# Performance work log

Hardware: AMD Instinct MI355X
Metric: run time of the kernel (lower is better)

The kernel has to match this reference:

```python
import jax, jax.numpy as jnp
import numpy as np

DIM = 256
DIM_HEAD = 32
HEADS = DIM // DIM_HEAD
SCALE = DIM_HEAD ** -0.5


def setup_inputs() -> dict:
    key = jax.random.key(0)
    ks = jax.random.split(key, 8)
    D1 = DIM + 1
    s = 1.0 / np.sqrt(D1)
    x = jax.random.normal(ks[0], (2, 32, 32, 8, 8, D1), dtype=jnp.float32)
    Wqv = jax.random.normal(ks[1], (D1, DIM), dtype=jnp.float32) * s
    Wkv = jax.random.normal(ks[2], (D1, DIM), dtype=jnp.float32) * s
    Wvv = jax.random.normal(ks[3], (D1, DIM), dtype=jnp.float32) * s
    Wqd = jax.random.normal(ks[4], (D1, 1), dtype=jnp.float32) * s
    Wkd = jax.random.normal(ks[5], (D1, 1), dtype=jnp.float32) * s
    Wvd = jax.random.normal(ks[6], (D1, 1), dtype=jnp.float32) * s
    Wout = jax.random.normal(ks[7], (D1, D1), dtype=jnp.float32) * s
    return {"x": x, "Wqv": Wqv, "Wkv": Wkv, "Wvv": Wvv,
            "Wqd": Wqd, "Wkd": Wkd, "Wvd": Wvd, "Wout": Wout}


def reference(x, Wqv, Wkv, Wvv, Wqd, Wkd, Wvd, Wout):
    b, gx, gy, w1, w2, D1 = x.shape
    B = b * gx * gy          # number of windows
    n = w1 * w2              # tokens per window
    h, dh = HEADS, DIM_HEAD
    xf = x.reshape(B, n, D1)

    def split_heads(t, nh, d):
        # (B, n, nh*d) -> (B, nh, n, d)
        return t.reshape(B, n, nh, d).transpose(0, 2, 1, 3)

    qv = split_heads(xf @ Wqv, h, dh) * SCALE
    kv = split_heads(xf @ Wkv, h, dh)
    vv = split_heads(xf @ Wvv, h, dh)
    qd = split_heads(xf @ Wqd, 1, 1) * SCALE
    kd = split_heads(xf @ Wkd, 1, 1)
    vd = split_heads(xf @ Wvd, 1, 1)

    sim_v = jnp.einsum('bhid,bhjd->bhij', qv, kv)          # (B, h, n, n)
    sim_d = jnp.einsum('bhid,bhjd->bhij', qd, kd)          # (B, 1, n, n)
    sim_m = sim_v * jax.nn.sigmoid(sim_d)                  # depth-gated scores

    attn_v = jax.nn.softmax(sim_m, axis=-1)                # (B, h, n, n)
    attn_d = jax.nn.softmax(jnp.sum(sim_m, axis=1, keepdims=True), axis=-1)  # (B,1,n,n)

    out_v = jnp.einsum('bhij,bhjd->bhid', attn_v, vv)      # (B, h, n, dh)
    out_d = jnp.einsum('bhij,bhjd->bhid', attn_d, vd)      # (B, 1, n, 1)

    out_v = out_v.transpose(0, 2, 1, 3).reshape(B, n, h * dh)  # (B, n, dim)
    out_d = out_d.transpose(0, 2, 1, 3).reshape(B, n, 1)       # (B, n, 1)

    out = jnp.concatenate([out_v, out_d], axis=-1) @ Wout      # (B, n, dim+1)
    return out.reshape(b, gx, gy, w1, w2, D1)
```

## Files before the change

kernel.cpp:

```cpp
#include <hip/hip_runtime.h>


#define D1    257
#define NTOK  64
#define KT    9
#define NT_CAT 49
#define NT_OUT 17
#define SCALE 0.17677669529663687f

#define XS2_OFF 0
#define QS2_OFF 36864
#define KS2_OFF 71680
#define VS2_OFF 104448
#define DS2_OFF 137216
#define QD2_OFF 153856
#define KD2_OFF 154112
#define VD2_OFF 154368
#define LDS2    154624
#define AT_STRIDE 68
#define DS_STRIDE 65

#define XS_OFF    0
#define XS_STRIDE 296
#define OC_STRIDE 296
#define QS_OFF    37888
#define QK_STRIDE 264
#define KS_OFF    72704
#define VS_OFF    106496
#define DS_OFF    139264
#define QD_OFF    155904
#define KD_OFF    156160
#define VD_OFF    156416
#define LDS_SIZE  156672

#define WCAT_ELEMS (KT * NT_CAT * 512)
#define WOUT_ELEMS (KT * NT_OUT * 512)
#define XWIN_ELEMS (36 * 512)

using bf16x8 = __attribute__((ext_vector_type(8))) short;
using s16x4  = __attribute__((ext_vector_type(4))) short;
using f32x4  = __attribute__((ext_vector_type(4))) float;

__device__ __forceinline__ short f2b(float f) {
  unsigned u = __float_as_uint(f);
  u = (u + 0x7FFFu + ((u >> 16) & 1u)) >> 16;
  return (short)u;
}

__device__ __forceinline__ f32x4 mfma16(bf16x8 a, bf16x8 b, f32x4 c) {
  return __builtin_amdgcn_mfma_f32_16x16x32_bf16(a, b, c, 0, 0, 0);
}

__global__ void prep_weights(const float* __restrict__ Wqv, const float* __restrict__ Wkv,
                             const float* __restrict__ Wvv, const float* __restrict__ Wqd,
                             const float* __restrict__ Wkd, const float* __restrict__ Wvd,
                             const float* __restrict__ Wout,
                             short* __restrict__ wcatp, short* __restrict__ woutp) {
  int idx = blockIdx.x * 256 + threadIdx.x;
  if (idx < WCAT_ELEMS) {
    int j = idx & 7, lane = (idx >> 3) & 63, rest = idx >> 9;
    int nt = rest % NT_CAT, kt = rest / NT_CAT;
    int k = 32 * kt + (lane >> 4) * 8 + j;
    int n = 16 * nt + (lane & 15);
    float v = 0.f;
    if (k < D1) {
      if (n < 256)       v = Wqv[k * 256 + n] * SCALE;
      else if (n < 512)  v = Wkv[k * 256 + (n - 256)];
      else if (n < 768)  v = Wvv[k * 256 + (n - 512)];
      else if (n == 768) v = Wqd[k] * SCALE;
      else if (n == 769) v = Wkd[k];
      else if (n == 770) v = Wvd[k];
    }
    wcatp[idx] = f2b(v);
  } else {
    int i2 = idx - WCAT_ELEMS;
    int j = i2 & 7, lane = (i2 >> 3) & 63, rest = i2 >> 9;
    int nt = rest % NT_OUT, kt = rest / NT_OUT;
    int k = 32 * kt + (lane >> 4) * 8 + j;
    int n = 16 * nt + (lane & 15);
    float v = (k < D1 && n < D1) ? Wout[k * D1 + n] : 0.f;
    woutp[i2] = f2b(v);
  }
}

__global__ void prep_x(const float* __restrict__ x, short* __restrict__ xbf, int win0) {
  int i = blockIdx.x * 256 + threadIdx.x;
  int widx = blockIdx.y;
  int j = i & 7, lane = (i >> 3) & 63, frag = i >> 9;
  int kt = frag >> 2, mt = frag & 3;
  int m = lane & 15, q = lane >> 4;
  int row = 16 * mt + m;
  int col = 32 * kt + 8 * q + j;
  float v = 0.f;
  if (col < D1)
    v = x[((size_t)(win0 + widx) * NTOK + row) * D1 + col];
  xbf[(size_t)widx * XWIN_ELEMS + i] = f2b(v);
}

__global__ __launch_bounds__(1024)
void vda_attn2(const short* __restrict__ xbf, const short* __restrict__ wcatp,
               const short* __restrict__ woutp, float* __restrict__ out, int win0) {
  extern __shared__ char smem[];
  short* xs   = (short*)(smem + XS2_OFF);
  short* qs   = (short*)(smem + QS2_OFF);
  short* ks   = (short*)(smem + KS2_OFF);
  short* vs   = (short*)(smem + VS2_OFF);
  float* dsum = (float*)(smem + DS2_OFF);
  float* qd_s = (float*)(smem + QD2_OFF);
  float* kd_s = (float*)(smem + KD2_OFF);
  float* vd_s = (float*)(smem + VD2_OFF);
  short* oc = xs;

  const int tid  = threadIdx.x;
  const int lane = tid & 63;
  const int w    = tid >> 6;
  const int m    = lane & 15;
  const int q    = lane >> 4;
  const int q8   = q * 8;
  const int widx = blockIdx.x;
  const int win  = win0 + widx;

  for (int i = tid; i < 64 * DS_STRIDE; i += 1024) dsum[i] = 0.f;
  {
    const int4* src = (const int4*)(xbf + (size_t)widx * XWIN_ELEMS);
    int4* dst = (int4*)xs;
    for (int i = tid; i < 2304; i += 1024) dst[i] = src[i];
  }
  __syncthreads();

  {
    f32x4 acc[4][4];
#pragma unroll
    for (int t = 0; t < 4; ++t)
#pragma unroll
      for (int mt = 0; mt < 4; ++mt) acc[t][mt] = f32x4{0.f, 0.f, 0.f, 0.f};

    for (int kt = 0; kt < KT; ++kt) {
      bf16x8 af[4];
#pragma unroll
      for (int mt = 0; mt < 4; ++mt)
        af[mt] = *(const bf16x8*)&xs[(kt * 4 + mt) * 512 + lane * 8];
#pragma unroll
      for (int t = 0; t < 4; ++t) {
        int nt = w + 16 * t;
        if (nt < NT_CAT) {
          bf16x8 bfr = *(const bf16x8*)(wcatp + ((size_t)(kt * NT_CAT + nt) * 64 + lane) * 8);
#pragma unroll
          for (int mt = 0; mt < 4; ++mt)
            acc[t][mt] = mfma16(af[mt], bfr, acc[t][mt]);
        }
      }
    }
    {
      int cq = (2 * w + (m >> 3)) & 3;
      int jj = m & 7;
      int fb = (w >> 1) * 4;
#pragma unroll
      for (int mt = 0; mt < 4; ++mt)
#pragma unroll
        for (int r = 0; r < 4; ++r)
          qs[(fb + mt) * 512 + (cq * 16 + 4 * q + r) * 8 + jj] = f2b(acc[0][mt][r]);
#pragma unroll
      for (int mt = 0; mt < 4; ++mt)
#pragma unroll
        for (int r = 0; r < 4; ++r)
          ks[(fb + mt) * 512 + (cq * 16 + 4 * q + r) * 8 + jj] = f2b(acc[1][mt][r]);
#pragma unroll
      for (int mt = 0; mt < 4; ++mt) {
        int frag = w * 2 + (mt >> 1);
        int q2 = (2 * mt + (q >> 1)) & 3;
        int j0 = 4 * (q & 1);
        s16x4 pk;
#pragma unroll
        for (int r = 0; r < 4; ++r) pk[r] = f2b(acc[2][mt][r]);
        *(s16x4*)&vs[frag * 512 + (q2 * 16 + m) * 8 + j0] = pk;
      }
      if (w == 0 && m < 3) {
        float* dst = (m == 0) ? qd_s : (m == 1) ? kd_s : vd_s;
#pragma unroll
        for (int mt = 0; mt < 4; ++mt)
#pragma unroll
          for (int r = 0; r < 4; ++r)
            dst[16 * mt + 4 * q + r] = acc[3][mt][r];
      }
    }
  }
  __syncthreads();

  const int rw = w & 3;
  const int hp = w >> 2;

  bf16x8 aq[2];
#pragma unroll
  for (int hh = 0; hh < 2; ++hh)
    aq[hh] = *(const bf16x8*)&qs[(((2 * hp + hh) * 4 + rw)) * 512 + lane * 8];

  float gate[4][4], ssum[4][4];
  {
    float qd_r[4], kd_c[4];
#pragma unroll
    for (int r = 0; r < 4; ++r) qd_r[r] = qd_s[16 * rw + 4 * q + r];
#pragma unroll
    for (int nt = 0; nt < 4; ++nt) kd_c[nt] = kd_s[16 * nt + m];
#pragma unroll
    for (int nt = 0; nt < 4; ++nt)
#pragma unroll
      for (int r = 0; r < 4; ++r) {
        float t = qd_r[r] * kd_c[nt];
        gate[nt][r] = 1.f / (1.f + __expf(-t));
        ssum[nt][r] = 0.f;
      }
  }
  __syncthreads();

  if (hp == 0) {
    int4 z4; z4.x = 0; z4.y = 0; z4.z = 0; z4.w = 0;
    ((int4*)(oc + 32 * 512))[rw * 64 + lane] = z4;
  }

  short* atw = (short*)(smem + QS2_OFF) + w * (16 * AT_STRIDE);

#pragma unroll
  for (int hh = 0; hh < 2; ++hh) {
    int h = 2 * hp + hh;
    f32x4 sv[4];
#pragma unroll
    for (int nt = 0; nt < 4; ++nt) {
      bf16x8 bk = *(const bf16x8*)&ks[(h * 4 + nt) * 512 + lane * 8];
      f32x4 z = {0.f, 0.f, 0.f, 0.f};
      sv[nt] = mfma16(aq[hh], bk, z);
    }
    float sm[4][4], mx[4], sum[4];
#pragma unroll
    for (int r = 0; r < 4; ++r) mx[r] = -3.4e38f;
#pragma unroll
    for (int nt = 0; nt < 4; ++nt)
#pragma unroll
      for (int r = 0; r < 4; ++r) {
        float s = sv[nt][r] * gate[nt][r];
        ssum[nt][r] += s;
        sm[nt][r] = s;
        mx[r] = fmaxf(mx[r], s);
      }
#pragma unroll
    for (int r = 0; r < 4; ++r) {
#pragma unroll
      for (int msk = 1; msk < 16; msk <<= 1)
        mx[r] = fmaxf(mx[r], __shfl_xor(mx[r], msk));
      sum[r] = 0.f;
    }
#pragma unroll
    for (int nt = 0; nt < 4; ++nt)
#pragma unroll
      for (int r = 0; r < 4; ++r) {
        float p = __expf(sm[nt][r] - mx[r]);
        sm[nt][r] = p;
        sum[r] += p;
      }
#pragma unroll
    for (int r = 0; r < 4; ++r) {
#pragma unroll
      for (int msk = 1; msk < 16; msk <<= 1)
        sum[r] += __shfl_xor(sum[r], msk);
      sum[r] = 1.f / sum[r];
    }
#pragma unroll
    for (int nt = 0; nt < 4; ++nt)
#pragma unroll
      for (int r = 0; r < 4; ++r)
        atw[(4 * q + r) * AT_STRIDE + 16 * nt + m] = f2b(sm[nt][r] * sum[r]);

    s16x4 l0 = *(const s16x4*)&atw[m * AT_STRIDE + q8];
    s16x4 l1 = *(const s16x4*)&atw[m * AT_STRIDE + q8 + 4];
    s16x4 l2 = *(const s16x4*)&atw[m * AT_STRIDE + 32 + q8];
    s16x4 l3 = *(const s16x4*)&atw[m * AT_STRIDE + 32 + q8 + 4];
    bf16x8 a0, a1;
#pragma unroll
    for (int j = 0; j < 4; ++j) { a0[j] = l0[j]; a0[4 + j] = l1[j]; a1[j] = l2[j]; a1[4 + j] = l3[j]; }

#pragma unroll
    for (int ntv = 0; ntv < 2; ++ntv) {
      bf16x8 bv0 = *(const bf16x8*)&vs[(((2 * h + ntv) * 2) + 0) * 512 + lane * 8];
      bf16x8 bv1 = *(const bf16x8*)&vs[(((2 * h + ntv) * 2) + 1) * 512 + lane * 8];
      f32x4 o = {0.f, 0.f, 0.f, 0.f};
      o = mfma16(a0, bv0, o);
      o = mfma16(a1, bv1, o);
      int cq2 = (2 * ntv + (m >> 3)) & 3;
#pragma unroll
      for (int r = 0; r < 4; ++r)
        oc[(h * 4 + rw) * 512 + (cq2 * 16 + 4 * q + r) * 8 + (m & 7)] = f2b(o[r]);
    }
  }

#pragma unroll
  for (int nt = 0; nt < 4; ++nt)
#pragma unroll
    for (int r = 0; r < 4; ++r)
      atomicAdd(&dsum[(16 * rw + 4 * q + r) * DS_STRIDE + 16 * nt + m], ssum[nt][r]);
  __syncthreads();

  if (hp == 0) {
    float sd[4][4], mx[4], sum[4];
#pragma unroll
    for (int nt = 0; nt < 4; ++nt)
#pragma unroll
      for (int r = 0; r < 4; ++r)
        sd[nt][r] = dsum[(16 * rw + 4 * q + r) * DS_STRIDE + 16 * nt + m];
#pragma unroll
    for (int r = 0; r < 4; ++r) mx[r] = -3.4e38f;
#pragma unroll
    for (int nt = 0; nt < 4; ++nt)
#pragma unroll
      for (int r = 0; r < 4; ++r) mx[r] = fmaxf(mx[r], sd[nt][r]);
#pragma unroll
    for (int r = 0; r < 4; ++r) {
#pragma unroll
      for (int msk = 1; msk < 16; msk <<= 1)
        mx[r] = fmaxf(mx[r], __shfl_xor(mx[r], msk));
      sum[r] = 0.f;
    }
#pragma unroll
    for (int nt = 0; nt < 4; ++nt)
#pragma unroll
      for (int r = 0; r < 4; ++r) {
        sd[nt][r] = __expf(sd[nt][r] - mx[r]);
        sum[r] += sd[nt][r];
      }
#pragma unroll
    for (int r = 0; r < 4; ++r) {
#pragma unroll
      for (int msk = 1; msk < 16; msk <<= 1)
        sum[r] += __shfl_xor(sum[r], msk);
      sum[r] = 1.f / sum[r];
    }
    float vd_c[4];
#pragma unroll
    for (int nt = 0; nt < 4; ++nt) vd_c[nt] = vd_s[16 * nt + m];
    float ov[4] = {0.f, 0.f, 0.f, 0.f};
#pragma unroll
    for (int nt = 0; nt < 4; ++nt)
#pragma unroll
      for (int r = 0; r < 4; ++r) ov[r] += sd[nt][r] * vd_c[nt];
#pragma unroll
    for (int r = 0; r < 4; ++r) {
#pragma unroll
      for (int msk = 1; msk < 16; msk <<= 1)
        ov[r] += __shfl_xor(ov[r], msk);
    }
    if (m == 0) {
#pragma unroll
      for (int r = 0; r < 4; ++r)
        oc[(32 + rw) * 512 + (4 * q + r) * 8] = f2b(ov[r] * sum[r]);
    }
  }
  __syncthreads();

  {
    f32x4 acc2[2][4];
#pragma unroll
    for (int t = 0; t < 2; ++t)
#pragma unroll
      for (int mt = 0; mt < 4; ++mt) acc2[t][mt] = f32x4{0.f, 0.f, 0.f, 0.f};

    for (int kt = 0; kt < KT; ++kt) {
      bf16x8 ao[4];
#pragma unroll
      for (int mt = 0; mt < 4; ++mt)
        ao[mt] = *(const bf16x8*)&oc[(kt * 4 + mt) * 512 + lane * 8];
#pragma unroll
      for (int t = 0; t < 2; ++t) {
        int nt = w + 16 * t;
        if (nt < NT_OUT) {
          bf16x8 bw = *(const bf16x8*)(woutp + ((size_t)(kt * NT_OUT + nt) * 64 + lane) * 8);
#pragma unroll
          for (int mt = 0; mt < 4; ++mt)
            acc2[t][mt] = mfma16(ao[mt], bw, acc2[t][mt]);
        }
      }
    }
#pragma unroll
    for (int t = 0; t < 2; ++t) {
      int nt = w + 16 * t;
      if (nt >= NT_OUT) continue;
      int n = 16 * nt + m;
      if (n < D1) {
#pragma unroll
        for (int mt = 0; mt < 4; ++mt)
#pragma unroll
          for (int r = 0; r < 4; ++r)
            out[((size_t)win * NTOK + 16 * mt + 4 * q + r) * D1 + n] = acc2[t][mt][r];
      }
    }
  }
}

__global__ __launch_bounds__(1024)
void vda_attn(const float* __restrict__ x, const short* __restrict__ wcatp,
              const short* __restrict__ woutp, float* __restrict__ out) {
  extern __shared__ char smem[];
  short* xs  = (short*)(smem + XS_OFF);
  short* qs  = (short*)(smem + QS_OFF);
  short* ks  = (short*)(smem + KS_OFF);
  short* vs  = (short*)(smem + VS_OFF);
  float* dsum = (float*)(smem + DS_OFF);
  float* qd_s = (float*)(smem + QD_OFF);
  float* kd_s = (float*)(smem + KD_OFF);
  float* vd_s = (float*)(smem + VD_OFF);
  short* oc = xs;

  const int tid  = threadIdx.x;
  const int lane = tid & 63;
  const int w    = tid >> 6;
  const int m    = lane & 15;
  const int q    = lane >> 4;
  const int q8   = q * 8;
  const int win  = blockIdx.x;

  for (int i = tid; i < 64 * 39; i += 1024) {
    int r = i / 39, c = 257 + (i % 39);
    xs[r * XS_STRIDE + c] = 0;
  }
  for (int i = tid; i < 64 * DS_STRIDE; i += 1024) dsum[i] = 0.f;
  {
    const float4* xw4 = (const float4*)(x + (size_t)win * (NTOK * D1));
    for (int f4 = tid; f4 < 4112; f4 += 1024) {
      float4 v = xw4[f4];
      float vals[4] = {v.x, v.y, v.z, v.w};
      int o0 = f4 * 4;
      int r0 = o0 / D1, c0 = o0 - r0 * D1;
#pragma unroll
      for (int jj = 0; jj < 4; ++jj) {
        int c = c0 + jj, r = r0;
        if (c >= D1) { c -= D1; r += 1; }
        xs[r * XS_STRIDE + c] = f2b(vals[jj]);
      }
    }
  }
  __syncthreads();

  {
    f32x4 acc[4][4];
#pragma unroll
    for (int t = 0; t < 4; ++t)
#pragma unroll
      for (int mt = 0; mt < 4; ++mt) acc[t][mt] = f32x4{0.f, 0.f, 0.f, 0.f};

    for (int kt = 0; kt < KT; ++kt) {
      bf16x8 af[4];
#pragma unroll
      for (int mt = 0; mt < 4; ++mt)
        af[mt] = *(const bf16x8*)&xs[(16 * mt + m) * XS_STRIDE + 32 * kt + q8];
#pragma unroll
      for (int t = 0; t < 4; ++t) {
        int nt = w + 16 * t;
        if (nt < NT_CAT) {
          bf16x8 bfr = *(const bf16x8*)(wcatp + ((size_t)(kt * NT_CAT + nt) * 64 + lane) * 8);
#pragma unroll
          for (int mt = 0; mt < 4; ++mt)
            acc[t][mt] = mfma16(af[mt], bfr, acc[t][mt]);
        }
      }
    }
#pragma unroll
    for (int t = 0; t < 4; ++t) {
      int nt = w + 16 * t;
      if (nt >= NT_CAT) continue;
      int c = nt * 16 + m;
      if (c < 256) {
#pragma unroll
        for (int mt = 0; mt < 4; ++mt)
#pragma unroll
          for (int r = 0; r < 4; ++r)
            qs[(16 * mt + 4 * q + r) * QK_STRIDE + c] = f2b(acc[t][mt][r]);
      } else if (c < 512) {
#pragma unroll
        for (int mt = 0; mt < 4; ++mt)
#pragma unroll
          for (int r = 0; r < 4; ++r)
            ks[(16 * mt + 4 * q + r) * QK_STRIDE + (c - 256)] = f2b(acc[t][mt][r]);
      } else if (c < 768) {
#pragma unroll
        for (int mt = 0; mt < 4; ++mt) {
          int frag = (nt - 32) * 2 + (mt >> 1);
          int q2 = (2 * mt + (q >> 1)) & 3;
          int j0 = 4 * (q & 1);
          s16x4 pk;
#pragma unroll
          for (int r = 0; r < 4; ++r) pk[r] = f2b(acc[t][mt][r]);
          *(s16x4*)&vs[frag * 512 + (q2 * 16 + m) * 8 + j0] = pk;
        }
      } else {
        if (m < 3) {
          float* dst = (m == 0) ? qd_s : (m == 1) ? kd_s : vd_s;
#pragma unroll
          for (int mt = 0; mt < 4; ++mt)
#pragma unroll
            for (int r = 0; r < 4; ++r)
              dst[16 * mt + 4 * q + r] = acc[t][mt][r];
        }
      }
    }
  }
  __syncthreads();

  const int rw = w & 3;
  const int hp = w >> 2;

  bf16x8 aq[2];
#pragma unroll
  for (int hh = 0; hh < 2; ++hh)
    aq[hh] = *(const bf16x8*)&qs[(16 * rw + m) * QK_STRIDE + 32 * (2 * hp + hh) + q8];

  float gate[4][4], ssum[4][4];
  {
    float qd_r[4], kd_c[4];
#pragma unroll
    for (int r = 0; r < 4; ++r) qd_r[r] = qd_s[16 * rw + 4 * q + r];
#pragma unroll
    for (int nt = 0; nt < 4; ++nt) kd_c[nt] = kd_s[16 * nt + m];
#pragma unroll
    for (int nt = 0; nt < 4; ++nt)
#pragma unroll
      for (int r = 0; r < 4; ++r) {
        float t = qd_r[r] * kd_c[nt];
        gate[nt][r] = 1.f / (1.f + __expf(-t));
        ssum[nt][r] = 0.f;
      }
  }
  __syncthreads();

  if (hp == 0) {
    bf16x8 z = {0, 0, 0, 0, 0, 0, 0, 0};
    *(bf16x8*)&oc[(16 * rw + m) * OC_STRIDE + 256 + q8] = z;
  }

  short* atw = (short*)(smem + QS_OFF) + w * (16 * AT_STRIDE);

#pragma unroll
  for (int hh = 0; hh < 2; ++hh) {
    int h = 2 * hp + hh;
    f32x4 sv[4];
#pragma unroll
    for (int nt = 0; nt < 4; ++nt) {
      bf16x8 bkf = *(const bf16x8*)&ks[(16 * nt + m) * QK_STRIDE + 32 * h + q8];
      f32x4 z = {0.f, 0.f, 0.f, 0.f};
      sv[nt] = mfma16(aq[hh], bkf, z);
    }
    float sm[4][4], mx[4], sum[4];
#pragma unroll
    for (int r = 0; r < 4; ++r) mx[r] = -3.4e38f;
#pragma unroll
    for (int nt = 0; nt < 4; ++nt)
#pragma unroll
      for (int r = 0; r < 4; ++r) {
        float s = sv[nt][r] * gate[nt][r];
        ssum[nt][r] += s;
        sm[nt][r] = s;
        mx[r] = fmaxf(mx[r], s);
      }
#pragma unroll
    for (int r = 0; r < 4; ++r) {
#pragma unroll
      for (int msk = 1; msk < 16; msk <<= 1)
        mx[r] = fmaxf(mx[r], __shfl_xor(mx[r], msk));
      sum[r] = 0.f;
    }
#pragma unroll
    for (int nt = 0; nt < 4; ++nt)
#pragma unroll
      for (int r = 0; r < 4; ++r) {
        float p = __expf(sm[nt][r] - mx[r]);
        sm[nt][r] = p;
        sum[r] += p;
      }
#pragma unroll
    for (int r = 0; r < 4; ++r) {
#pragma unroll
      for (int msk = 1; msk < 16; msk <<= 1)
        sum[r] += __shfl_xor(sum[r], msk);
      sum[r] = 1.f / sum[r];
    }
#pragma unroll
    for (int nt = 0; nt < 4; ++nt)
#pragma unroll
      for (int r = 0; r < 4; ++r)
        atw[(4 * q + r) * AT_STRIDE + 16 * nt + m] = f2b(sm[nt][r] * sum[r]);

    s16x4 l0 = *(const s16x4*)&atw[m * AT_STRIDE + q8];
    s16x4 l1 = *(const s16x4*)&atw[m * AT_STRIDE + q8 + 4];
    s16x4 l2 = *(const s16x4*)&atw[m * AT_STRIDE + 32 + q8];
    s16x4 l3 = *(const s16x4*)&atw[m * AT_STRIDE + 32 + q8 + 4];
    bf16x8 a0, a1;
#pragma unroll
    for (int j = 0; j < 4; ++j) { a0[j] = l0[j]; a0[4 + j] = l1[j]; a1[j] = l2[j]; a1[4 + j] = l3[j]; }

#pragma unroll
    for (int ntp = 0; ntp < 2; ++ntp) {
      bf16x8 bv0 = *(const bf16x8*)&vs[(((2 * h + ntp) * 2) + 0) * 512 + lane * 8];
      bf16x8 bv1 = *(const bf16x8*)&vs[(((2 * h + ntp) * 2) + 1) * 512 + lane * 8];
      f32x4 o = {0.f, 0.f, 0.f, 0.f};
      o = mfma16(a0, bv0, o);
      o = mfma16(a1, bv1, o);
#pragma unroll
      for (int r = 0; r < 4; ++r)
        oc[(16 * rw + 4 * q + r) * OC_STRIDE + 32 * h + 16 * ntp + m] = f2b(o[r]);
    }
  }

#pragma unroll
  for (int nt = 0; nt < 4; ++nt)
#pragma unroll
    for (int r = 0; r < 4; ++r)
      atomicAdd(&dsum[(16 * rw + 4 * q + r) * DS_STRIDE + 16 * nt + m], ssum[nt][r]);
  __syncthreads();

  if (hp == 0) {
    float sd[4][4], mx[4], sum[4];
#pragma unroll
    for (int nt = 0; nt < 4; ++nt)
#pragma unroll
      for (int r = 0; r < 4; ++r)
        sd[nt][r] = dsum[(16 * rw + 4 * q + r) * DS_STRIDE + 16 * nt + m];
#pragma unroll
    for (int r = 0; r < 4; ++r) mx[r] = -3.4e38f;
#pragma unroll
    for (int nt = 0; nt < 4; ++nt)
#pragma unroll
      for (int r = 0; r < 4; ++r) mx[r] = fmaxf(mx[r], sd[nt][r]);
#pragma unroll
    for (int r = 0; r < 4; ++r) {
#pragma unroll
      for (int msk = 1; msk < 16; msk <<= 1)
        mx[r] = fmaxf(mx[r], __shfl_xor(mx[r], msk));
      sum[r] = 0.f;
    }
#pragma unroll
    for (int nt = 0; nt < 4; ++nt)
#pragma unroll
      for (int r = 0; r < 4; ++r) {
        sd[nt][r] = __expf(sd[nt][r] - mx[r]);
        sum[r] += sd[nt][r];
      }
#pragma unroll
    for (int r = 0; r < 4; ++r) {
#pragma unroll
      for (int msk = 1; msk < 16; msk <<= 1)
        sum[r] += __shfl_xor(sum[r], msk);
      sum[r] = 1.f / sum[r];
    }
    float vd_c[4];
#pragma unroll
    for (int nt = 0; nt < 4; ++nt) vd_c[nt] = vd_s[16 * nt + m];
    float ov[4] = {0.f, 0.f, 0.f, 0.f};
#pragma unroll
    for (int nt = 0; nt < 4; ++nt)
#pragma unroll
      for (int r = 0; r < 4; ++r) ov[r] += sd[nt][r] * vd_c[nt];
#pragma unroll
    for (int r = 0; r < 4; ++r) {
#pragma unroll
      for (int msk = 1; msk < 16; msk <<= 1)
        ov[r] += __shfl_xor(ov[r], msk);
    }
    if (m == 0) {
#pragma unroll
      for (int r = 0; r < 4; ++r)
        oc[(16 * rw + 4 * q + r) * OC_STRIDE + 256] = f2b(ov[r] * sum[r]);
    }
  }
  __syncthreads();

  {
    f32x4 acc2[2][4];
#pragma unroll
    for (int t = 0; t < 2; ++t)
#pragma unroll
      for (int mt = 0; mt < 4; ++mt) acc2[t][mt] = f32x4{0.f, 0.f, 0.f, 0.f};

    for (int kt = 0; kt < KT; ++kt) {
      bf16x8 ao[4];
#pragma unroll
      for (int mt = 0; mt < 4; ++mt)
        ao[mt] = *(const bf16x8*)&oc[(16 * mt + m) * OC_STRIDE + 32 * kt + q8];
#pragma unroll
      for (int t = 0; t < 2; ++t) {
        int nt = w + 16 * t;
        if (nt < NT_OUT) {
          bf16x8 bw = *(const bf16x8*)(woutp + ((size_t)(kt * NT_OUT + nt) * 64 + lane) * 8);
#pragma unroll
          for (int mt = 0; mt < 4; ++mt)
            acc2[t][mt] = mfma16(ao[mt], bw, acc2[t][mt]);
        }
      }
    }
#pragma unroll
    for (int t = 0; t < 2; ++t) {
      int nt = w + 16 * t;
      if (nt >= NT_OUT) continue;
      int n = 16 * nt + m;
      if (n < D1) {
#pragma unroll
        for (int mt = 0; mt < 4; ++mt)
#pragma unroll
          for (int r = 0; r < 4; ++r)
            out[((size_t)win * NTOK + 16 * mt + 4 * q + r) * D1 + n] = acc2[t][mt][r];
      }
    }
  }
}

extern "C" void kernel_launch(void* const* d_in, const int* in_sizes, int n_in,
                              void* d_out, int out_size, void* d_ws, size_t ws_size,
                              hipStream_t stream) {
  (void)n_in; (void)out_size;
  const float* x    = (const float*)d_in[0];
  const float* Wqv  = (const float*)d_in[1];
  const float* Wkv  = (const float*)d_in[2];
  const float* Wvv  = (const float*)d_in[3];
  const float* Wqd  = (const float*)d_in[4];
  const float* Wkd  = (const float*)d_in[5];
  const float* Wvd  = (const float*)d_in[6];
  const float* Wout = (const float*)d_in[7];
  float* out = (float*)d_out;

  short* wcatp = (short*)d_ws;
  short* woutp = wcatp + WCAT_ELEMS;

  int nwin = in_sizes[0] / (NTOK * D1);

  int prep_blocks = (WCAT_ELEMS + WOUT_ELEMS) / 256;
  prep_weights<<<prep_blocks, 256, 0, stream>>>(Wqv, Wkv, Wvv, Wqd, Wkd, Wvd, Wout, wcatp, woutp);

  const size_t woff = (size_t)(WCAT_ELEMS + WOUT_ELEMS) * 2;
  const size_t per_win = (size_t)XWIN_ELEMS * 2;
  size_t avail = (ws_size > woff) ? ws_size - woff : 0;
  long long cwll = (long long)(avail / per_win);
  int cw = (cwll > nwin) ? nwin : (int)cwll;

  if (cw < 128) {
    hipFuncSetAttribute((const void*)vda_attn, hipFuncAttributeMaxDynamicSharedMemorySize, LDS_SIZE);
    vda_attn<<<nwin, 1024, LDS_SIZE, stream>>>(x, wcatp, woutp, out);
    return;
  }

  hipFuncSetAttribute((const void*)vda_attn2, hipFuncAttributeMaxDynamicSharedMemorySize, LDS2);
  short* xbf = (short*)((char*)d_ws + woff);

  for (int base = 0; base < nwin; base += cw) {
    int g = nwin - base;
    if (g > cw) g = cw;
    prep_x<<<dim3(72, g), 256, 0, stream>>>(x, xbf, base);
    vda_attn2<<<g, 1024, LDS2, stream>>>(xbf, wcatp, woutp, out, base);
  }
}
```

Baseline: 619.5 us.

## Software-pipeline weight and activation fragment loads in projection GEMMs; grid-stride prep_x

The QKV and output projection loops now prefetch weight fragments two k-steps ahead and activation fragments one step ahead in registers, with the first weight loads issued before the LDS staging barrier. The QKV projection is split into two passes (Q/K tiles, then V/depth tiles) to cut live accumulator registers. The final store of the out-of-range output tile is specialised to a single column. prep_x becomes a fixed-size grid-stride kernel over windows instead of a 2D grid. The goal is to hide global load latency behind MFMA work, at the cost of reading the x tile from LDS twice and added register pressure from prefetch buffers.

```diff
diff --git a/kernel.cpp b/kernel.cpp
--- a/kernel.cpp
+++ b/kernel.cpp
@@ -50,6 +50,9 @@
 __device__ __forceinline__ f32x4 mfma16(bf16x8 a, bf16x8 b, f32x4 c) {
   return __builtin_amdgcn_mfma_f32_16x16x32_bf16(a, b, c, 0, 0, 0);
 }
+
+#define WFRAG(kt, nt) (*(const bf16x8*)(wcatp + ((size_t)((kt) * NT_CAT + (nt)) * 64 + lane) * 8))
+#define OFRAG(kt, nt) (*(const bf16x8*)(woutp + ((size_t)((kt) * NT_OUT + (nt)) * 64 + lane) * 8))
 
 __global__ void prep_weights(const float* __restrict__ Wqv, const float* __restrict__ Wkv,
                              const float* __restrict__ Wvv, const float* __restrict__ Wqd,
@@ -83,18 +86,21 @@
   }
 }
 
-__global__ void prep_x(const float* __restrict__ x, short* __restrict__ xbf, int win0) {
-  int i = blockIdx.x * 256 + threadIdx.x;
-  int widx = blockIdx.y;
-  int j = i & 7, lane = (i >> 3) & 63, frag = i >> 9;
-  int kt = frag >> 2, mt = frag & 3;
-  int m = lane & 15, q = lane >> 4;
-  int row = 16 * mt + m;
-  int col = 32 * kt + 8 * q + j;
-  float v = 0.f;
-  if (col < D1)
-    v = x[((size_t)(win0 + widx) * NTOK + row) * D1 + col];
-  xbf[(size_t)widx * XWIN_ELEMS + i] = f2b(v);
+#define PX_WSTEP 28
+__global__ __launch_bounds__(256)
+void prep_x(const float* __restrict__ x, short* __restrict__ xbf, int win0, int nw) {
+  const int e = (blockIdx.x % 72) * 256 + threadIdx.x;
+  const int j = e & 7, lane = (e >> 3) & 63, frag = e >> 9;
+  const int kt = frag >> 2, mt = frag & 3;
+  const int m = lane & 15, q = lane >> 4;
+  const int row = 16 * mt + m;
+  const int col = 32 * kt + 8 * q + j;
+  const bool valid = (col < D1);
+  const size_t xoff = (size_t)row * D1 + col;
+  for (int widx = blockIdx.x / 72; widx < nw; widx += PX_WSTEP) {
+    float v = valid ? x[(size_t)(win0 + widx) * (NTOK * D1) + xoff] : 0.f;
+    xbf[(size_t)widx * XWIN_ELEMS + e] = f2b(v);
+  }
 }
 
 __global__ __launch_bounds__(1024)
@@ -120,37 +126,57 @@
   const int widx = blockIdx.x;
   const int win  = win0 + widx;
 
-  for (int i = tid; i < 64 * DS_STRIDE; i += 1024) dsum[i] = 0.f;
+  bf16x8 bA0 = WFRAG(0, w),      bA1 = WFRAG(1, w);
+  bf16x8 bB0 = WFRAG(0, w + 16), bB1 = WFRAG(1, w + 16);
+
   {
     const int4* src = (const int4*)(xbf + (size_t)widx * XWIN_ELEMS);
     int4* dst = (int4*)xs;
     for (int i = tid; i < 2304; i += 1024) dst[i] = src[i];
   }
+  for (int i = tid; i < 64 * DS_STRIDE; i += 1024) dsum[i] = 0.f;
   __syncthreads();
 
   {
-    f32x4 acc[4][4];
-#pragma unroll
-    for (int t = 0; t < 4; ++t)
+    f32x4 acc[2][4];
+#pragma unroll
+    for (int t = 0; t < 2; ++t)
 #pragma unroll
       for (int mt = 0; mt < 4; ++mt) acc[t][mt] = f32x4{0.f, 0.f, 0.f, 0.f};
 
+    bf16x8 a_c[4];
+#pragma unroll
+    for (int mt = 0; mt < 4; ++mt)
+      a_c[mt] = *(const bf16x8*)&xs[mt * 512 + lane * 8];
+
+#pragma unroll
     for (int kt = 0; kt < KT; ++kt) {
-      bf16x8 af[4];
-#pragma unroll
-      for (int mt = 0; mt < 4; ++mt)
-        af[mt] = *(const bf16x8*)&xs[(kt * 4 + mt) * 512 + lane * 8];
-#pragma unroll
-      for (int t = 0; t < 4; ++t) {
-        int nt = w + 16 * t;
-        if (nt < NT_CAT) {
-          bf16x8 bfr = *(const bf16x8*)(wcatp + ((size_t)(kt * NT_CAT + nt) * 64 + lane) * 8);
-#pragma unroll
-          for (int mt = 0; mt < 4; ++mt)
-            acc[t][mt] = mfma16(af[mt], bfr, acc[t][mt]);
-        }
-      }
-    }
+      bf16x8 bA2{}, bB2{};
+      if (kt + 2 < KT) {
+        bA2 = WFRAG(kt + 2, w);
+        bB2 = WFRAG(kt + 2, w + 16);
+      }
+      bf16x8 a_n[4];
+      if (kt + 1 < KT) {
+#pragma unroll
+        for (int mt = 0; mt < 4; ++mt)
+          a_n[mt] = *(const bf16x8*)&xs[((kt + 1) * 4 + mt) * 512 + lane * 8];
+      }
+#pragma unroll
+      for (int mt = 0; mt < 4; ++mt) acc[0][mt] = mfma16(a_c[mt], bA0, acc[0][mt]);
+#pragma unroll
+      for (int mt = 0; mt < 4; ++mt) acc[1][mt] = mfma16(a_c[mt], bB0, acc[1][mt]);
+      bA0 = bA1; bA1 = bA2; bB0 = bB1; bB1 = bB2;
+      if (kt + 1 < KT) {
+#pragma unroll
+        for (int mt = 0; mt < 4; ++mt) a_c[mt] = a_n[mt];
+      }
+    }
+
+    bf16x8 cA0 = WFRAG(0, w + 32), cA1 = WFRAG(1, w + 32);
+    bf16x8 cB0{}, cB1{};
+    if (w == 0) { cB0 = WFRAG(0, 48); cB1 = WFRAG(1, 48); }
+
     {
       int cq = (2 * w + (m >> 3)) & 3;
       int jj = m & 7;
@@ -165,24 +191,60 @@
 #pragma unroll
         for (int r = 0; r < 4; ++r)
           ks[(fb + mt) * 512 + (cq * 16 + 4 * q + r) * 8 + jj] = f2b(acc[1][mt][r]);
-#pragma unroll
-      for (int mt = 0; mt < 4; ++mt) {
-        int frag = w * 2 + (mt >> 1);
-        int q2 = (2 * mt + (q >> 1)) & 3;
-        int j0 = 4 * (q & 1);
-        s16x4 pk;
-#pragma unroll
-        for (int r = 0; r < 4; ++r) pk[r] = f2b(acc[2][mt][r]);
-        *(s16x4*)&vs[frag * 512 + (q2 * 16 + m) * 8 + j0] = pk;
-      }
-      if (w == 0 && m < 3) {
-        float* dst = (m == 0) ? qd_s : (m == 1) ? kd_s : vd_s;
+    }
+
+#pragma unroll
+    for (int t = 0; t < 2; ++t)
+#pragma unroll
+      for (int mt = 0; mt < 4; ++mt) acc[t][mt] = f32x4{0.f, 0.f, 0.f, 0.f};
+
+#pragma unroll
+    for (int mt = 0; mt < 4; ++mt)
+      a_c[mt] = *(const bf16x8*)&xs[mt * 512 + lane * 8];
+
+#pragma unroll
+    for (int kt = 0; kt < KT; ++kt) {
+      bf16x8 cA2{}, cB2{};
+      if (kt + 2 < KT) {
+        cA2 = WFRAG(kt + 2, w + 32);
+        if (w == 0) cB2 = WFRAG(kt + 2, 48);
+      }
+      bf16x8 a_n[4];
+      if (kt + 1 < KT) {
 #pragma unroll
         for (int mt = 0; mt < 4; ++mt)
-#pragma unroll
-          for (int r = 0; r < 4; ++r)
-            dst[16 * mt + 4 * q + r] = acc[3][mt][r];
-      }
+          a_n[mt] = *(const bf16x8*)&xs[((kt + 1) * 4 + mt) * 512 + lane * 8];
+      }
+#pragma unroll
+      for (int mt = 0; mt < 4; ++mt) acc[0][mt] = mfma16(a_c[mt], cA0, acc[0][mt]);
+      if (w == 0) {
+#pragma unroll
+        for (int mt = 0; mt < 4; ++mt) acc[1][mt] = mfma16(a_c[mt], cB0, acc[1][mt]);
+      }
+      cA0 = cA1; cA1 = cA2; cB0 = cB1; cB1 = cB2;
+      if (kt + 1 < KT) {
+#pragma unroll
+        for (int mt = 0; mt < 4; ++mt) a_c[mt] = a_n[mt];
+      }
+    }
+
+#pragma unroll
+    for (int mt = 0; mt < 4; ++mt) {
+      int frag = w * 2 + (mt >> 1);
+      int q2 = (2 * mt + (q >> 1)) & 3;
+      int j0 = 4 * (q & 1);
+      s16x4 pk;
+#pragma unroll
+      for (int r = 0; r < 4; ++r) pk[r] = f2b(acc[0][mt][r]);
+      *(s16x4*)&vs[frag * 512 + (q2 * 16 + m) * 8 + j0] = pk;
+    }
+    if (w == 0 && m < 3) {
+      float* dst = (m == 0) ? qd_s : (m == 1) ? kd_s : vd_s;
+#pragma unroll
+      for (int mt = 0; mt < 4; ++mt)
+#pragma unroll
+        for (int r = 0; r < 4; ++r)
+          dst[16 * mt + 4 * q + r] = acc[1][mt][r];
     }
   }
   __syncthreads();
@@ -353,6 +415,10 @@
         oc[(32 + rw) * 512 + (4 * q + r) * 8] = f2b(ov[r] * sum[r]);
     }
   }
+
+  bf16x8 dA0 = OFRAG(0, w), dA1 = OFRAG(1, w);
+  bf16x8 dB0{}, dB1{};
+  if (w == 0) { dB0 = OFRAG(0, 16); dB1 = OFRAG(1, 16); }
   __syncthreads();
 
   {
@@ -362,34 +428,51 @@
 #pragma unroll
       for (int mt = 0; mt < 4; ++mt) acc2[t][mt] = f32x4{0.f, 0.f, 0.f, 0.f};
 
+    bf16x8 ao_c[4];
+#pragma unroll
+    for (int mt = 0; mt < 4; ++mt)
+      ao_c[mt] = *(const bf16x8*)&oc[mt * 512 + lane * 8];
+
+#pragma unroll
     for (int kt = 0; kt < KT; ++kt) {
-      bf16x8 ao[4];
+      bf16x8 dA2{}, dB2{};
+      if (kt + 2 < KT) {
+        dA2 = OFRAG(kt + 2, w);
+        if (w == 0) dB2 = OFRAG(kt + 2, 16);
+      }
+      bf16x8 ao_n[4];
+      if (kt + 1 < KT) {
+#pragma unroll
+        for (int mt = 0; mt < 4; ++mt)
+          ao_n[mt] = *(const bf16x8*)&oc[((kt + 1) * 4 + mt) * 512 + lane * 8];
+      }
+#pragma unroll
+      for (int mt = 0; mt < 4; ++mt) acc2[0][mt] = mfma16(ao_c[mt], dA0, acc2[0][mt]);
+      if (w == 0) {
+#pragma unroll
+        for (int mt = 0; mt < 4; ++mt) acc2[1][mt] = mfma16(ao_c[mt], dB0, acc2[1][mt]);
+      }
+      dA0 = dA1; dA1 = dA2; dB0 = dB1; dB1 = dB2;
+      if (kt + 1 < KT) {
+#pragma unroll
+        for (int mt = 0; mt < 4; ++mt) ao_c[mt] = ao_n[mt];
+      }
+    }
+
+    {
+      int n = 16 * w + m;
 #pragma unroll
       for (int mt = 0; mt < 4; ++mt)
-        ao[mt] = *(const bf16x8*)&oc[(kt * 4 + mt) * 512 + lane * 8];
-#pragma unroll
-      for (int t = 0; t < 2; ++t) {
-        int nt = w + 16 * t;
-        if (nt < NT_OUT) {
-          bf16x8 bw = *(const bf16x8*)(woutp + ((size_t)(kt * NT_OUT + nt) * 64 + lane) * 8);
-#pragma unroll
-          for (int mt = 0; mt < 4; ++mt)
-            acc2[t][mt] = mfma16(ao[mt], bw, acc2[t][mt]);
-        }
-      }
-    }
-#pragma unroll
-    for (int t = 0; t < 2; ++t) {
-      int nt = w + 16 * t;
-      if (nt >= NT_OUT) continue;
-      int n = 16 * nt + m;
-      if (n < D1) {
-#pragma unroll
-        for (int mt = 0; mt < 4; ++mt)
-#pragma unroll
-          for (int r = 0; r < 4; ++r)
-            out[((size_t)win * NTOK + 16 * mt + 4 * q + r) * D1 + n] = acc2[t][mt][r];
-      }
+#pragma unroll
+        for (int r = 0; r < 4; ++r)
+          out[((size_t)win * NTOK + 16 * mt + 4 * q + r) * D1 + n] = acc2[0][mt][r];
+    }
+    if (w == 0 && m == 0) {
+#pragma unroll
+      for (int mt = 0; mt < 4; ++mt)
+#pragma unroll
+        for (int r = 0; r < 4; ++r)
+          out[((size_t)win * NTOK + 16 * mt + 4 * q + r) * D1 + 256] = acc2[1][mt][r];
     }
   }
 }
@@ -749,7 +832,7 @@
   for (int base = 0; base < nwin; base += cw) {
     int g = nwin - base;
     if (g > cw) g = cw;
-    prep_x<<<dim3(72, g), 256, 0, stream>>>(x, xbf, base);
+    prep_x<<<72 * PX_WSTEP, 256, 0, stream>>>(x, xbf, base, g);
     vda_attn2<<<g, 1024, LDS2, stream>>>(xbf, wcatp, woutp, out, base);
   }
 }
```

Result: faster. 576.5 us (-6.9%).
